# Performance work log

Hardware: AMD Instinct MI355X
Metric: run time of the kernel (lower is better)

## Reference

```python
import jax, jax.numpy as jnp
import numpy as np

B, N, DIM, H, E = 2, 2048, 1024, 16, 8
HD = DIM // H
SCALE = HD ** -0.5


def setup_inputs() -> dict:
    key = jax.random.key(0)
    ks = jax.random.split(key, 6)
    s = DIM ** -0.5
    return {
        "x": jax.random.normal(ks[0], (B, N, DIM), dtype=jnp.float32),
        "w_qkv": jax.random.normal(ks[1], (3 * DIM, DIM), dtype=jnp.float32) * s,
        "b_qkv": jnp.zeros((3 * DIM,), dtype=jnp.float32),
        "w_proj": jax.random.normal(ks[2], (DIM, DIM), dtype=jnp.float32) * s,
        "b_proj": jnp.zeros((DIM,), dtype=jnp.float32),
        "rel_pos": jax.random.normal(ks[3], (1, H, E, E), dtype=jnp.float32),
    }


def reference(x, w_qkv, b_qkv, w_proj, b_proj, rel_pos):
    tpe = N // E  # tokens per entity (tile count)
    # qkv: [B,N,3*DIM] -> [3,B,H,N,HD]
    qkv = (jnp.einsum("bnc,dc->bnd", x, w_qkv) + b_qkv)
    qkv = qkv.reshape(B, N, 3, H, HD).transpose(2, 0, 3, 1, 4)
    q, k, v = qkv[0], qkv[1], qkv[2]
    attn = jnp.einsum("bhnd,bhmd->bhnm", q, k) * SCALE
    # torch .repeat tiles the ExE bias: bias[i,j] = rel_pos[i % E, j % E]
    rel_bias = jnp.tile(rel_pos, (B, 1, tpe, tpe))
    attn = jax.nn.softmax(attn + rel_bias, axis=-1)
    out = jnp.einsum("bhnm,bhmd->bhnd", attn, v)
    out = out.transpose(0, 2, 1, 3).reshape(B, N, DIM)
    return jnp.einsum("bnc,dc->bnd", out, w_proj) + b_proj
```

## Files before the change

### kernel.cpp

```cpp
#include <hip/hip_runtime.h>
#include <hip/hip_bf16.h>
#include <stdint.h>

#define B_ 2
#define N_ 2048
#define DIM_ 1024
#define H_ 16
#define HD_ 64
#define NT_ 32

typedef __attribute__((ext_vector_type(8))) short short8;
typedef __attribute__((ext_vector_type(4))) float f32x4;
typedef __attribute__((ext_vector_type(16))) float f32x16;

__device__ __forceinline__ unsigned short f2bf(float f) {
  __bf16 h = (__bf16)f;
  return __builtin_bit_cast(unsigned short, h);
}

__device__ __forceinline__ void gload_lds16(const void* g, void* l) {
  __builtin_amdgcn_global_load_lds(
      (const __attribute__((address_space(1))) unsigned int*)g,
      (__attribute__((address_space(3))) unsigned int*)l,
      16, 0, 0);
}

#define XN4_ 1048576
#define WQ4_ 786432
__global__ __launch_bounds__(256) void cvt_all_kernel(
    const float4* __restrict__ x, const float4* __restrict__ wq,
    const float4* __restrict__ wp,
    ushort4* __restrict__ xb, ushort4* __restrict__ wqb, ushort4* __restrict__ wpb) {
  int i = blockIdx.x * 256 + threadIdx.x;
  const float4* src;
  ushort4* dst;
  if (i < XN4_) {
    src = x + i; dst = xb + i;
  } else if (i < XN4_ + WQ4_) {
    src = wq + (i - XN4_); dst = wqb + (i - XN4_);
  } else {
    src = wp + (i - XN4_ - WQ4_); dst = wpb + (i - XN4_ - WQ4_);
  }
  float4 v = *src;
  ushort4 o;
  o.x = f2bf(v.x); o.y = f2bf(v.y); o.z = f2bf(v.z); o.w = f2bf(v.w);
  *dst = o;
}

__device__ __forceinline__ void gemm128_mainloop(
    const ushort* __restrict__ A, const ushort* __restrict__ Bw, int K,
    int bm, int bn, ushort* As, ushort* Bs, f32x4 acc[4][4]) {
  const int tid = threadIdx.x;
  const int lane = tid & 63;
  const int w = tid >> 6, wr = w >> 1, wc = w & 1;
  const int fr = lane & 15, fq = lane >> 4;
  const int srow = tid >> 3, scol = (tid & 7) * 8;

  const ushort* Ag = A + (size_t)(bm * 128 + srow) * K + scol;
  const ushort* Bg = Bw + (size_t)(bn * 128 + srow) * K + scol;
  ushort* Asd = As + tid * 8;
  ushort* Bsd = Bs + tid * 8;

  for (int kt = 0; kt < K; kt += 64) {
    __syncthreads();
#pragma unroll
    for (int c = 0; c < 4; ++c) {
      gload_lds16(Ag + (size_t)(c * 32) * K + kt, Asd + c * 2048);
      gload_lds16(Bg + (size_t)(c * 32) * K + kt, Bsd + c * 2048);
    }
    __syncthreads();

    short8 af[2][4], bf[2][4];
#pragma unroll
    for (int kk = 0; kk < 2; ++kk) {
#pragma unroll
      for (int mi = 0; mi < 4; ++mi)
        af[kk][mi] = *(const short8*)&As[(wr * 64 + mi * 16 + fr) * 64 + kk * 32 + fq * 8];
#pragma unroll
      for (int ni = 0; ni < 4; ++ni)
        bf[kk][ni] = *(const short8*)&Bs[(wc * 64 + ni * 16 + fr) * 64 + kk * 32 + fq * 8];
    }
#pragma unroll
    for (int kk = 0; kk < 2; ++kk)
#pragma unroll
      for (int mi = 0; mi < 4; ++mi)
#pragma unroll
        for (int ni = 0; ni < 4; ++ni)
          acc[mi][ni] = __builtin_amdgcn_mfma_f32_16x16x32_bf16(
              af[kk][mi], bf[kk][ni], acc[mi][ni], 0, 0, 0);
  }
}

__global__ __launch_bounds__(256) void gemm_qkv_kernel(
    const ushort* __restrict__ xb, const ushort* __restrict__ wqkv,
    const float* __restrict__ bqkv,
    ushort* __restrict__ qo, ushort* __restrict__ ko, ushort* __restrict__ vo) {
  __shared__ ushort As[128 * 64];
  __shared__ ushort Bs[128 * 64];
  f32x4 acc[4][4] = {};
  const int bn = blockIdx.x, bm = blockIdx.y;
  gemm128_mainloop(xb, wqkv, DIM_, bm, bn, As, Bs, acc);

  const int tid = threadIdx.x, lane = tid & 63;
  const int w = tid >> 6, wr = w >> 1, wc = w & 1;
  const int fr = lane & 15, fq = lane >> 4;
#pragma unroll
  for (int mi = 0; mi < 4; ++mi) {
#pragma unroll
    for (int ni = 0; ni < 4; ++ni) {
      int col = bn * 128 + wc * 64 + ni * 16 + fr;
      int i3 = col >> 10, h = (col >> 6) & 15, hd = col & 63;
      float bias = bqkv[col];
      int m0 = bm * 128 + wr * 64 + mi * 16 + fq * 4;
      int b = m0 >> 11, n = m0 & 2047;
      if (i3 == 2) {
        ushort4 o;
        o.x = f2bf(acc[mi][ni][0] + bias);
        o.y = f2bf(acc[mi][ni][1] + bias);
        o.z = f2bf(acc[mi][ni][2] + bias);
        o.w = f2bf(acc[mi][ni][3] + bias);
        *(ushort4*)&vo[((size_t)((b * H_ + h) * HD_ + hd)) * N_ + n] = o;
      } else {
        ushort* base = (i3 == 0) ? qo : ko;
#pragma unroll
        for (int r = 0; r < 4; ++r)
          base[((size_t)(b * H_ + h) * N_ + n + r) * HD_ + hd] = f2bf(acc[mi][ni][r] + bias);
      }
    }
  }
}

__global__ __launch_bounds__(256) void gemm_proj_kernel(
    const ushort* __restrict__ ao, const ushort* __restrict__ wp,
    const float* __restrict__ bp, float* __restrict__ out) {
  __shared__ ushort As[128 * 64];
  __shared__ ushort Bs[128 * 64];
  f32x4 acc[4][4] = {};
  const int bn = blockIdx.x, bm = blockIdx.y;
  gemm128_mainloop(ao, wp, DIM_, bm, bn, As, Bs, acc);

  const int tid = threadIdx.x, lane = tid & 63;
  const int w = tid >> 6, wr = w >> 1, wc = w & 1;
  const int fr = lane & 15, fq = lane >> 4;
#pragma unroll
  for (int mi = 0; mi < 4; ++mi) {
#pragma unroll
    for (int ni = 0; ni < 4; ++ni) {
      int col = bn * 128 + wc * 64 + ni * 16 + fr;
      float bias = bp[col];
#pragma unroll
      for (int r = 0; r < 4; ++r) {
        int m = bm * 128 + wr * 64 + mi * 16 + fq * 4 + r;
        out[(size_t)m * DIM_ + col] = acc[mi][ni][r] + bias;
      }
    }
  }
}

__global__ __launch_bounds__(256, 2) void attn_kernel(
    const ushort* __restrict__ Qg, const ushort* __restrict__ Kg,
    const ushort* __restrict__ Vtg, const float* __restrict__ rel,
    ushort* __restrict__ outb) {
  __shared__ ushort Ks[2][64 * 64];
  __shared__ ushort Vs[2][64 * 64];

  const int bid = blockIdx.x;
  const int xcd = bid & 7, idx = bid >> 3;
  const int bh = xcd * 4 + (idx >> 4);
  const int q0 = (idx & 15) * 128;
  const int h = bh & 15;
  const int tid = threadIdx.x, lane = tid & 63, w = tid >> 6;
  const int ql = lane & 31, hi = lane >> 5;

  const float LOG2E = 1.4426950408889634f;
  const float SB = 0.125f * LOG2E;

  float bias2[4];
#pragma unroll
  for (int r = 0; r < 4; ++r)
    bias2[r] = rel[h * 64 + (ql & 7) * 8 + r + 4 * hi] * LOG2E;

  const ushort* qrow = Qg + ((size_t)bh * N_ + q0 + w * 32 + ql) * HD_;
  short8 qf[4];
#pragma unroll
  for (int kk = 0; kk < 4; ++kk)
    qf[kk] = *(const short8*)&qrow[kk * 16 + hi * 8];

  float l = 0.f;
  f32x16 oacc[2] = {};
  f32x16 sA[2], sB[2];

  const int srow = tid >> 3, scol = (tid & 7) * 8;
  const int swsrc = scol ^ ((srow & 7) << 3);
  int kcol[4];
#pragma unroll
  for (int kk = 0; kk < 4; ++kk)
    kcol[kk] = (kk * 16 + hi * 8) ^ ((ql & 7) << 3);

#define STAGE_K(t, bb)                                                              \
  {                                                                                 \
    const size_t kv0 = (size_t)(t) * 64;                                            \
    _Pragma("unroll") for (int c = 0; c < 2; ++c)                                   \
        gload_lds16(Kg + ((size_t)bh * N_ + kv0 + c * 32 + srow) * HD_ + swsrc,     \
                    &Ks[bb][c * 2048 + tid * 8]);                                   \
  }
#define STAGE_V(t, bb)                                                              \
  {                                                                                 \
    const size_t kv0 = (size_t)(t) * 64;                                            \
    _Pragma("unroll") for (int c = 0; c < 2; ++c)                                   \
        gload_lds16(Vtg + ((size_t)(bh * HD_ + c * 32 + srow)) * N_ + kv0 + swsrc,  \
                    &Vs[bb][c * 2048 + tid * 8]);                                   \
  }

#define QKT(S, K_)                                                                  \
  {                                                                                 \
    _Pragma("unroll") for (int z = 0; z < 16; ++z) { S[0][z] = 0.f; S[1][z] = 0.f; }\
    __builtin_amdgcn_s_setprio(1);                                                  \
    _Pragma("unroll") for (int kk = 0; kk < 4; ++kk) {                              \
      short8 kf0 = *(const short8*)&(K_)[ql * 64 + kcol[kk]];                       \
      short8 kf1 = *(const short8*)&(K_)[(32 + ql) * 64 + kcol[kk]];                \
      S[0] = __builtin_amdgcn_mfma_f32_32x32x16_bf16(kf0, qf[kk], S[0], 0, 0, 0);   \
      S[1] = __builtin_amdgcn_mfma_f32_32x32x16_bf16(kf1, qf[kk], S[1], 0, 0, 0);   \
    }                                                                               \
    __builtin_amdgcn_s_setprio(0);                                                  \
  }

#define SOFTPV(S, V_)                                                               \
  {                                                                                 \
    float rs = 0.f;                                                                 \
    uint32_t c[2][8];                                                               \
    _Pragma("unroll") for (int blk = 0; blk < 2; ++blk) {                           \
      _Pragma("unroll") for (int i = 0; i < 8; ++i) {                               \
        float pa = __builtin_amdgcn_exp2f(S[blk][2 * i] * SB + bias2[(2 * i) & 3]); \
        float pb = __builtin_amdgcn_exp2f(S[blk][2 * i + 1] * SB + bias2[(2 * i + 1) & 3]); \
        rs += pa + pb;                                                              \
        c[blk][i] = ((uint32_t)f2bf(pb) << 16) | f2bf(pa);                          \
      }                                                                             \
    }                                                                               \
    rs += __shfl_xor(rs, 32, 64);                                                   \
    l += rs;                                                                        \
    _Pragma("unroll") for (int blk = 0; blk < 2; ++blk) {                           \
      asm("v_permlane32_swap_b32 %0, %1" : "+v"(c[blk][0]), "+v"(c[blk][2]));       \
      asm("v_permlane32_swap_b32 %0, %1" : "+v"(c[blk][1]), "+v"(c[blk][3]));       \
      asm("v_permlane32_swap_b32 %0, %1" : "+v"(c[blk][4]), "+v"(c[blk][6]));       \
      asm("v_permlane32_swap_b32 %0, %1" : "+v"(c[blk][5]), "+v"(c[blk][7]));       \
    }                                                                               \
    __builtin_amdgcn_s_setprio(1);                                                  \
    _Pragma("unroll") for (int kk = 0; kk < 4; ++kk) {                              \
      union { uint32_t u[4]; short8 s8; } pb_;                                      \
      pb_.u[0] = c[kk >> 1][(kk & 1) * 4 + 0];                                      \
      pb_.u[1] = c[kk >> 1][(kk & 1) * 4 + 1];                                      \
      pb_.u[2] = c[kk >> 1][(kk & 1) * 4 + 2];                                      \
      pb_.u[3] = c[kk >> 1][(kk & 1) * 4 + 3];                                      \
      _Pragma("unroll") for (int db = 0; db < 2; ++db) {                            \
        short8 vf = *(const short8*)&(V_)[(db * 32 + ql) * 64 + kcol[kk]];          \
        oacc[db] = __builtin_amdgcn_mfma_f32_32x32x16_bf16(vf, pb_.s8, oacc[db], 0, 0, 0); \
      }                                                                             \
    }                                                                               \
    __builtin_amdgcn_s_setprio(0);                                                  \
  }

  STAGE_K(0, 0);
  STAGE_V(0, 0);
  __syncthreads();
  QKT(sA, Ks[0]);
  STAGE_K(1, 1);
  __syncthreads();

#pragma unroll 1
  for (int tt = 0; tt < 15; ++tt) {
    const int t = 2 * tt;
    STAGE_K(t + 2, 0);
    STAGE_V(t + 1, 1);
    QKT(sB, Ks[1]);
    SOFTPV(sA, Vs[0]);
    __syncthreads();
    STAGE_K(t + 3, 1);
    STAGE_V(t + 2, 0);
    QKT(sA, Ks[0]);
    SOFTPV(sB, Vs[1]);
    __syncthreads();
  }
  STAGE_V(31, 1);
  QKT(sB, Ks[1]);
  SOFTPV(sA, Vs[0]);
  __syncthreads();
  SOFTPV(sB, Vs[1]);

  const int b = bh >> 4;
  const float invl = 1.0f / l;
  const size_t rowbase = ((size_t)(b * N_ + q0 + w * 32 + ql)) * DIM_ + h * HD_;
#pragma unroll
  for (int db = 0; db < 2; ++db)
#pragma unroll
    for (int g = 0; g < 4; ++g) {
      ushort4 o;
      o.x = f2bf(oacc[db][4 * g + 0] * invl);
      o.y = f2bf(oacc[db][4 * g + 1] * invl);
      o.z = f2bf(oacc[db][4 * g + 2] * invl);
      o.w = f2bf(oacc[db][4 * g + 3] * invl);
      *(ushort4*)&outb[rowbase + db * 32 + 8 * g + 4 * hi] = o;
    }
#undef STAGE_K
#undef STAGE_V
#undef QKT
#undef SOFTPV
}

extern "C" void kernel_launch(void* const* d_in, const int* in_sizes, int n_in,
                              void* d_out, int out_size, void* d_ws, size_t ws_size,
                              hipStream_t stream) {
  const float* x      = (const float*)d_in[0];
  const float* w_qkv  = (const float*)d_in[1];
  const float* b_qkv  = (const float*)d_in[2];
  const float* w_proj = (const float*)d_in[3];
  const float* b_proj = (const float*)d_in[4];
  const float* rel    = (const float*)d_in[5];

  char* ws = (char*)d_ws;
  ushort* xb     = (ushort*)(ws + 0);
  ushort* wqkvb  = (ushort*)(ws + 8388608);
  ushort* wprojb = (ushort*)(ws + 14680064);
  ushort* qb     = (ushort*)(ws + 16777216);
  ushort* kb     = (ushort*)(ws + 25165824);
  ushort* vb     = (ushort*)(ws + 33554432);
  ushort* aob    = (ushort*)(ws + 41943040);
  (void)in_sizes; (void)n_in; (void)out_size; (void)ws_size;

  cvt_all_kernel<<<8192, 256, 0, stream>>>(
      (const float4*)x, (const float4*)w_qkv, (const float4*)w_proj,
      (ushort4*)xb, (ushort4*)wqkvb, (ushort4*)wprojb);

  gemm_qkv_kernel<<<dim3(24, 32), 256, 0, stream>>>(xb, wqkvb, b_qkv, qb, kb, vb);
  attn_kernel<<<512, 256, 0, stream>>>(qb, kb, vb, rel, aob);
  gemm_proj_kernel<<<dim3(8, 32), 256, 0, stream>>>(aob, wprojb, b_proj, (float*)d_out);
}
```

Measured before the change: 137.8 us.

## Fold softmax scale into Q, preload bias into MFMA accumulator, vectorize GEMM epilogues

Q is now pre-scaled by the softmax scale times log2e in the QKV epilogue, and the per-tile relative-position bias is loaded as the initial accumulator of the QK^T MFMA. This removes the per-element multiply-add before exp2 in the attention inner loop. The GEMM operand order is swapped so each lane holds four consecutive columns, which allows float4 bias loads and vectorized stores for Q, K and the projection output. V's transposed stores become scalar, and rounding Q to bf16 after scaling slightly changes numerics.

```diff
diff --git a/kernel.cpp b/kernel.cpp
--- a/kernel.cpp
+++ b/kernel.cpp
@@ -12,6 +12,9 @@
 typedef __attribute__((ext_vector_type(8))) short short8;
 typedef __attribute__((ext_vector_type(4))) float f32x4;
 typedef __attribute__((ext_vector_type(16))) float f32x16;
+
+#define LOG2E_ 1.4426950408889634f
+#define SBF_ (0.125f * LOG2E_)
 
 __device__ __forceinline__ unsigned short f2bf(float f) {
   __bf16 h = (__bf16)f;
@@ -87,7 +90,7 @@
 #pragma unroll
         for (int ni = 0; ni < 4; ++ni)
           acc[mi][ni] = __builtin_amdgcn_mfma_f32_16x16x32_bf16(
-              af[kk][mi], bf[kk][ni], acc[mi][ni], 0, 0, 0);
+              bf[kk][ni], af[kk][mi], acc[mi][ni], 0, 0, 0);
   }
 }
 
@@ -106,25 +109,30 @@
   const int fr = lane & 15, fq = lane >> 4;
 #pragma unroll
   for (int mi = 0; mi < 4; ++mi) {
+    int ng = bm * 128 + wr * 64 + mi * 16 + fr;
+    int b = ng >> 11, n = ng & 2047;
 #pragma unroll
     for (int ni = 0; ni < 4; ++ni) {
-      int col = bn * 128 + wc * 64 + ni * 16 + fr;
-      int i3 = col >> 10, h = (col >> 6) & 15, hd = col & 63;
-      float bias = bqkv[col];
-      int m0 = bm * 128 + wr * 64 + mi * 16 + fq * 4;
-      int b = m0 >> 11, n = m0 & 2047;
+      int colb = bn * 128 + wc * 64 + ni * 16 + fq * 4;
+      float4 b4 = *(const float4*)&bqkv[colb];
+      int i3 = colb >> 10, h = (colb >> 6) & 15, hdq = colb & 63;
+      float v0 = acc[mi][ni][0] + b4.x;
+      float v1 = acc[mi][ni][1] + b4.y;
+      float v2 = acc[mi][ni][2] + b4.z;
+      float v3 = acc[mi][ni][3] + b4.w;
       if (i3 == 2) {
+        size_t base = ((size_t)((b * H_ + h) * HD_ + hdq)) * N_ + n;
+        vo[base]          = f2bf(v0);
+        vo[base + N_]     = f2bf(v1);
+        vo[base + 2 * N_] = f2bf(v2);
+        vo[base + 3 * N_] = f2bf(v3);
+      } else {
+        const float s = (i3 == 0) ? SBF_ : 1.0f;
+        ushort* base = (i3 == 0) ? qo : ko;
         ushort4 o;
-        o.x = f2bf(acc[mi][ni][0] + bias);
-        o.y = f2bf(acc[mi][ni][1] + bias);
-        o.z = f2bf(acc[mi][ni][2] + bias);
-        o.w = f2bf(acc[mi][ni][3] + bias);
-        *(ushort4*)&vo[((size_t)((b * H_ + h) * HD_ + hd)) * N_ + n] = o;
-      } else {
-        ushort* base = (i3 == 0) ? qo : ko;
-#pragma unroll
-        for (int r = 0; r < 4; ++r)
-          base[((size_t)(b * H_ + h) * N_ + n + r) * HD_ + hd] = f2bf(acc[mi][ni][r] + bias);
+        o.x = f2bf(v0 * s); o.y = f2bf(v1 * s);
+        o.z = f2bf(v2 * s); o.w = f2bf(v3 * s);
+        *(ushort4*)&base[((size_t)(b * H_ + h) * N_ + n) * HD_ + hdq] = o;
       }
     }
   }
@@ -144,15 +152,17 @@
   const int fr = lane & 15, fq = lane >> 4;
 #pragma unroll
   for (int mi = 0; mi < 4; ++mi) {
+    int mg = bm * 128 + wr * 64 + mi * 16 + fr;
 #pragma unroll
     for (int ni = 0; ni < 4; ++ni) {
-      int col = bn * 128 + wc * 64 + ni * 16 + fr;
-      float bias = bp[col];
-#pragma unroll
-      for (int r = 0; r < 4; ++r) {
-        int m = bm * 128 + wr * 64 + mi * 16 + fq * 4 + r;
-        out[(size_t)m * DIM_ + col] = acc[mi][ni][r] + bias;
-      }
+      int colb = bn * 128 + wc * 64 + ni * 16 + fq * 4;
+      float4 b4 = *(const float4*)&bp[colb];
+      float4 o;
+      o.x = acc[mi][ni][0] + b4.x;
+      o.y = acc[mi][ni][1] + b4.y;
+      o.z = acc[mi][ni][2] + b4.z;
+      o.w = acc[mi][ni][3] + b4.w;
+      *(float4*)&out[(size_t)mg * DIM_ + colb] = o;
     }
   }
 }
@@ -172,13 +182,17 @@
   const int tid = threadIdx.x, lane = tid & 63, w = tid >> 6;
   const int ql = lane & 31, hi = lane >> 5;
 
-  const float LOG2E = 1.4426950408889634f;
-  const float SB = 0.125f * LOG2E;
-
-  float bias2[4];
-#pragma unroll
-  for (int r = 0; r < 4; ++r)
-    bias2[r] = rel[h * 64 + (ql & 7) * 8 + r + 4 * hi] * LOG2E;
+  f32x16 biasC;
+  {
+    float b0 = rel[h * 64 + (ql & 7) * 8 + 0 + 4 * hi] * LOG2E_;
+    float b1 = rel[h * 64 + (ql & 7) * 8 + 1 + 4 * hi] * LOG2E_;
+    float b2 = rel[h * 64 + (ql & 7) * 8 + 2 + 4 * hi] * LOG2E_;
+    float b3 = rel[h * 64 + (ql & 7) * 8 + 3 + 4 * hi] * LOG2E_;
+#pragma unroll
+    for (int z = 0; z < 16; z += 4) {
+      biasC[z] = b0; biasC[z + 1] = b1; biasC[z + 2] = b2; biasC[z + 3] = b3;
+    }
+  }
 
   const ushort* qrow = Qg + ((size_t)bh * N_ + q0 + w * 32 + ql) * HD_;
   short8 qf[4];
@@ -214,7 +228,8 @@
 
 #define QKT(S, K_)                                                                  \
   {                                                                                 \
-    _Pragma("unroll") for (int z = 0; z < 16; ++z) { S[0][z] = 0.f; S[1][z] = 0.f; }\
+    S[0] = biasC;                                                                   \
+    S[1] = biasC;                                                                   \
     __builtin_amdgcn_s_setprio(1);                                                  \
     _Pragma("unroll") for (int kk = 0; kk < 4; ++kk) {                              \
       short8 kf0 = *(const short8*)&(K_)[ql * 64 + kcol[kk]];                       \
@@ -227,16 +242,17 @@
 
 #define SOFTPV(S, V_)                                                               \
   {                                                                                 \
-    float rs = 0.f;                                                                 \
+    float rs_[4] = {0.f, 0.f, 0.f, 0.f};                                            \
     uint32_t c[2][8];                                                               \
     _Pragma("unroll") for (int blk = 0; blk < 2; ++blk) {                           \
       _Pragma("unroll") for (int i = 0; i < 8; ++i) {                               \
-        float pa = __builtin_amdgcn_exp2f(S[blk][2 * i] * SB + bias2[(2 * i) & 3]); \
-        float pb = __builtin_amdgcn_exp2f(S[blk][2 * i + 1] * SB + bias2[(2 * i + 1) & 3]); \
-        rs += pa + pb;                                                              \
+        float pa = __builtin_amdgcn_exp2f(S[blk][2 * i]);                           \
+        float pb = __builtin_amdgcn_exp2f(S[blk][2 * i + 1]);                       \
+        rs_[i & 3] += pa + pb;                                                      \
         c[blk][i] = ((uint32_t)f2bf(pb) << 16) | f2bf(pa);                          \
       }                                                                             \
     }                                                                               \
+    float rs = (rs_[0] + rs_[1]) + (rs_[2] + rs_[3]);                               \
     rs += __shfl_xor(rs, 32, 64);                                                   \
     l += rs;                                                                        \
     _Pragma("unroll") for (int blk = 0; blk < 2; ++blk) {                           \
```

Result: no change. 135.1 us, median of 5 (-1.9%).
